# Kernel tuning notes

Measured on AMD Instinct MI355X. Metric: run time of the kernel, lower is better.

Reference implementation:

```python
import jax, jax.numpy as jnp
import numpy as np

N_HEADS = 8
EPS = 1e-6


def setup_inputs() -> dict:
    key = jax.random.key(0)
    k1, k2, k3, k4, k5 = jax.random.split(key, 5)
    C_in, C_out = 512, 512
    x = jax.random.normal(k1, (4, C_in, 128, 128), dtype=jnp.float32)
    # Linear layers: torch stores weight as (out, in); init ~ U(-1/sqrt(in), 1/sqrt(in))
    s_in = 1.0 / np.sqrt(C_in)
    w_qkv = jax.random.uniform(k2, (3 * C_in, C_in), minval=-s_in, maxval=s_in, dtype=jnp.float32)
    b_qkv = jax.random.uniform(k3, (3 * C_in,), minval=-s_in, maxval=s_in, dtype=jnp.float32)
    w_out = jax.random.uniform(k4, (C_out, C_in), minval=-s_in, maxval=s_in, dtype=jnp.float32)
    b_out = jax.random.uniform(k5, (C_out,), minval=-s_in, maxval=s_in, dtype=jnp.float32)
    return {"x": x, "w_qkv": w_qkv, "b_qkv": b_qkv, "w_out": w_out, "b_out": b_out}


def reference(x, w_qkv, b_qkv, w_out, b_out):
    B, C = x.shape[0], x.shape[1]
    spatial = x.shape[2:]
    c = C // N_HEADS  # channels per head
    # features_last=False: move channels to last, flatten spatial -> (B, N, C)
    xl = jnp.moveaxis(x, 1, -1).reshape(B, -1, C)
    N = xl.shape[1]
    qkv = xl @ w_qkv.T + b_qkv  # (B, N, 3*C)
    # einops '(qkv head channels)': qkv outermost, then head, then channels
    qkv = qkv.reshape(B, N, 3, N_HEADS, c)
    q = jax.nn.relu(qkv[:, :, 0])  # (B, N, H, c)
    k = jax.nn.relu(qkv[:, :, 1])
    v = qkv[:, :, 2]
    # Associativity: value @ key^T @ query == value @ (key^T @ query).
    # kq[b,h,c,d] = sum_n k[b,n,h,c] * q[b,n,h,d]  -> small (c x c) per head
    kq = jnp.einsum('bnhc,bnhd->bhcd', k, q)
    vkq = jnp.einsum('bnhc,bhcd->bnhd', v, kq)  # (B, N, H, c)
    # Padded ones-row of value corresponds to column-sum of kq over axis c
    norm = kq.sum(axis=2)[:, None] + EPS  # (B, 1, H, c)
    attn = vkq / norm  # (B, N, H, c)
    # torch: (B,H,N,c).moveaxis(1,-1) -> (B,N,c,H); flatten(-2) -> (B,N,c*H)
    attn = jnp.transpose(attn, (0, 1, 3, 2)).reshape(B, N, -1)
    out = attn @ w_out.T + b_out  # (B, N, C_out)
    out = out.reshape(B, *spatial, -1)
    out = jnp.moveaxis(out, -1, 1)  # (B, C_out, *spatial)
    return out
```

## Files before the change

### kernel.cpp

```cpp
#include <hip/hip_runtime.h>
#include <hip/hip_bf16.h>
#include <stdint.h>

#define NSP 16384
#define BATCH 4
#define EPSV 1e-6f

typedef __attribute__((ext_vector_type(8))) short fragAB;
typedef __attribute__((ext_vector_type(4))) float fragC;

__device__ __forceinline__ unsigned short f2bf(float f) {
    union { float f; unsigned u; } un; un.f = f;
    unsigned r = un.u + 0x7fffu + ((un.u >> 16) & 1u);
    return (unsigned short)(r >> 16);
}

__device__ __forceinline__ float bf2f(unsigned u) {
    union { unsigned u; float f; } x; x.u = u << 16; return x.f;
}

#define GLD_LDS(g, l) __builtin_amdgcn_global_load_lds( \
    (const __attribute__((address_space(1))) void*)(g), \
    (__attribute__((address_space(3))) void*)(l), 16, 0, 0)

__device__ __forceinline__ fragAB ldfrag(const unsigned short* ls, int m, int g) {
    return *(const fragAB*)&ls[((m >> 3) << 9) + ((m & 7) << 6) + ((g ^ (m & 7)) << 3)];
}

__device__ __forceinline__ int tidx(int ch, int g) {
    return (ch << 7) + ((g ^ (ch & 7)) << 3);
}

__global__ __launch_bounds__(256) void transpose_prep(
    const float* __restrict__ x, unsigned short* __restrict__ xt,
    const float* __restrict__ wqkv, unsigned short* __restrict__ wqb,
    unsigned short* __restrict__ wvT) {
    __shared__ float lds[64 * 65];
    const int blk = blockIdx.x;
    const int t   = threadIdx.x;
    if (blk < 8192) {
        const int b  = blk >> 11;
        const int c0 = ((blk >> 8) & 7) * 64;
        const int n0 = (blk & 255) * 64;
        const int nl = (t & 15) * 4;
        const int cl = t >> 4;
#pragma unroll
        for (int i = 0; i < 4; ++i) {
            int c = cl + i * 16;
            float4 v = *(const float4*)&x[((size_t)(b * 512 + c0 + c)) * NSP + n0 + nl];
            float* row = &lds[c * 65 + nl];
            row[0] = v.x; row[1] = v.y; row[2] = v.z; row[3] = v.w;
        }
        __syncthreads();
#pragma unroll
        for (int i = 0; i < 2; ++i) {
            int ch = t + i * 256;
            int n  = ch >> 3;
            int co = (ch & 7) * 8;
            unsigned v0, v1, v2, v3;
            v0 = f2bf(lds[(co + 0) * 65 + n]) | ((unsigned)f2bf(lds[(co + 1) * 65 + n]) << 16);
            v1 = f2bf(lds[(co + 2) * 65 + n]) | ((unsigned)f2bf(lds[(co + 3) * 65 + n]) << 16);
            v2 = f2bf(lds[(co + 4) * 65 + n]) | ((unsigned)f2bf(lds[(co + 5) * 65 + n]) << 16);
            v3 = f2bf(lds[(co + 6) * 65 + n]) | ((unsigned)f2bf(lds[(co + 7) * 65 + n]) << 16);
            uint4 pk; pk.x = v0; pk.y = v1; pk.z = v2; pk.w = v3;
            *(uint4*)&xt[((size_t)(b * NSP + n0 + n)) * 512 + c0 + co] = pk;
        }
        return;
    }
    const int pblk = blk - 8192;
    if (pblk < 512) {
        int i = (pblk * 256 + t) * 4;
        float4 v = *(const float4*)&wqkv[i];
        uint2 pk;
        pk.x = f2bf(v.x) | ((unsigned)f2bf(v.y) << 16);
        pk.y = f2bf(v.z) | ((unsigned)f2bf(v.w) << 16);
        *(uint2*)&wqb[i] = pk;
        return;
    }
    const int c0  = ((pblk - 512) & 7) * 64;
    const int ch0 = ((pblk - 512) >> 3) * 64;
    const int cl  = (t & 15) * 4;
    const int rl  = t >> 4;
#pragma unroll
    for (int i = 0; i < 4; ++i) {
        int r = rl + i * 16;
        float4 v = *(const float4*)&wqkv[((size_t)(1024 + ch0 + r)) * 512 + c0 + cl];
        float* row = &lds[r * 65 + cl];
        row[0] = v.x; row[1] = v.y; row[2] = v.z; row[3] = v.w;
    }
    __syncthreads();
#pragma unroll
    for (int i = 0; i < 2; ++i) {
        int idx = t + i * 256;
        int c = idx >> 3;
        int g = (idx & 7) * 8;
        unsigned v0, v1, v2, v3;
        v0 = f2bf(lds[(g + 0) * 65 + c]) | ((unsigned)f2bf(lds[(g + 1) * 65 + c]) << 16);
        v1 = f2bf(lds[(g + 2) * 65 + c]) | ((unsigned)f2bf(lds[(g + 3) * 65 + c]) << 16);
        v2 = f2bf(lds[(g + 4) * 65 + c]) | ((unsigned)f2bf(lds[(g + 5) * 65 + c]) << 16);
        v3 = f2bf(lds[(g + 6) * 65 + c]) | ((unsigned)f2bf(lds[(g + 7) * 65 + c]) << 16);
        uint4 pk; pk.x = v0; pk.y = v1; pk.z = v2; pk.w = v3;
        *(uint4*)&wvT[((size_t)(c0 + c)) * 512 + ch0 + g] = pk;
    }
}

__global__ __launch_bounds__(256, 2) void gemm_qk_kq(
    const unsigned short* __restrict__ xt, const unsigned short* __restrict__ wq,
    const float* __restrict__ bqkv, unsigned short* __restrict__ partb) {
    __shared__ unsigned short S[(128 + 256) * 64];
    __shared__ unsigned short Qt[128 * 128];
    unsigned short* Bls = &S[8192];
    unsigned short* Kt  = &S[0];

    const int b  = blockIdx.z;
    const int hc = blockIdx.y;
    const int bx = blockIdx.x;
    const int n0 = bx * 128;
    const int t  = threadIdx.x;
    const int wv = t >> 6, ln = t & 63;
    const unsigned short* Ag = xt + (size_t)(b * NSP + n0) * 512;
    const int srow = ln >> 3;
    const int scol = ((ln & 7) ^ srow) << 3;
    const int isK = wv >> 1;
    unsigned short* T = isK ? Kt : Qt;

    fragC acc[8][4];
#pragma unroll
    for (int i = 0; i < 8; ++i)
#pragma unroll
        for (int j = 0; j < 4; ++j) { acc[i][j][0]=0.f; acc[i][j][1]=0.f; acc[i][j][2]=0.f; acc[i][j][3]=0.f; }

    for (int k0 = 0; k0 < 512; k0 += 64) {
#pragma unroll
        for (int i = 0; i < 4; ++i) {
            int ca = wv * 4 + i;
            GLD_LDS(Ag + (size_t)(ca * 8 + srow) * 512 + k0 + scol, &S[ca * 512]);
        }
#pragma unroll
        for (int i = 0; i < 8; ++i) {
            int cb = wv * 8 + i;
            int jl = cb * 8 + srow;
            int rg = hc * 128 + jl + ((jl & 128) ? 384 : 0);
            GLD_LDS(wq + (size_t)rg * 512 + k0 + scol, &Bls[cb * 512]);
        }
        __syncthreads();
#pragma unroll
        for (int kk = 0; kk < 64; kk += 32) {
            int g = (kk >> 3) + (ln >> 4);
            fragAB bf[4];
#pragma unroll
            for (int nt = 0; nt < 4; ++nt) bf[nt] = ldfrag(Bls, wv * 64 + nt * 16 + (ln & 15), g);
#pragma unroll
            for (int mt = 0; mt < 8; ++mt) {
                fragAB a = ldfrag(S, mt * 16 + (ln & 15), g);
#pragma unroll
                for (int nt = 0; nt < 4; ++nt)
                    acc[mt][nt] = __builtin_amdgcn_mfma_f32_16x16x32_bf16(a, bf[nt], acc[mt][nt], 0, 0, 0);
            }
        }
        __syncthreads();
    }

#pragma unroll
    for (int nt = 0; nt < 4; ++nt) {
        int chl = (wv & 1) * 64 + nt * 16 + (ln & 15);
        float bias = bqkv[hc * 128 + chl + (isK ? 512 : 0)];
#pragma unroll
        for (int mt = 0; mt < 8; ++mt) {
            int nb = mt * 16 + (ln >> 4) * 4;
            float r0 = acc[mt][nt][0] + bias; r0 = r0 > 0.f ? r0 : 0.f;
            float r1 = acc[mt][nt][1] + bias; r1 = r1 > 0.f ? r1 : 0.f;
            float r2 = acc[mt][nt][2] + bias; r2 = r2 > 0.f ? r2 : 0.f;
            float r3 = acc[mt][nt][3] + bias; r3 = r3 > 0.f ? r3 : 0.f;
            uint2 pk;
            pk.x = f2bf(r0) | ((unsigned)f2bf(r1) << 16);
            pk.y = f2bf(r2) | ((unsigned)f2bf(r3) << 16);
            int g = nb >> 3, o = nb & 7;
            *(uint2*)&T[tidx(chl, g) + o] = pk;
        }
    }
    __syncthreads();

    {
        const int wm = wv >> 1, wn = wv & 1;
        fragC ak[2][4];
#pragma unroll
        for (int i = 0; i < 2; ++i)
#pragma unroll
            for (int j = 0; j < 4; ++j) { ak[i][j][0]=0.f; ak[i][j][1]=0.f; ak[i][j][2]=0.f; ak[i][j][3]=0.f; }
#pragma unroll
        for (int kk = 0; kk < 128; kk += 32) {
            int g = (kk >> 3) + (ln >> 4);
            fragAB qf[4];
#pragma unroll
            for (int dt = 0; dt < 4; ++dt)
                qf[dt] = *(const fragAB*)&Qt[tidx(wm * 64 + dt * 16 + (ln & 15), g)];
#pragma unroll
            for (int ct = 0; ct < 2; ++ct) {
                fragAB kf = *(const fragAB*)&Kt[tidx(wm * 64 + wn * 32 + ct * 16 + (ln & 15), g)];
#pragma unroll
                for (int dt = 0; dt < 4; ++dt)
                    ak[ct][dt] = __builtin_amdgcn_mfma_f32_16x16x32_bf16(qf[dt], kf, ak[ct][dt], 0, 0, 0);
            }
        }
        unsigned short* pb = partb + ((size_t)((b * 8 + hc * 2 + wm) * 128 + bx)) * 4096
                           + wn * 2048 + ln * 4;
#pragma unroll
        for (int ct = 0; ct < 2; ++ct)
#pragma unroll
            for (int dt = 0; dt < 4; ++dt) {
                uint2 pk;
                pk.x = f2bf(ak[ct][dt][0]) | ((unsigned)f2bf(ak[ct][dt][1]) << 16);
                pk.y = f2bf(ak[ct][dt][2]) | ((unsigned)f2bf(ak[ct][dt][3]) << 16);
                *(uint2*)&pb[ct * 1024 + dt * 256] = pk;
            }
    }
}

__global__ __launch_bounds__(256) void reduce_kq(const unsigned short* __restrict__ partb,
                                                 float* __restrict__ kq) {
    const int tid = blockIdx.x * 256 + threadIdx.x;
    const int bh  = tid >> 10;
    const int s   = tid & 1023;
    const int off = s * 4;
    const unsigned short* p = partb + (size_t)bh * 128 * 4096 + off;
    float s0 = 0.f, s1 = 0.f, s2 = 0.f, s3 = 0.f;
#pragma unroll 4
    for (int blk = 0; blk < 128; ++blk) {
        uint2 v = *(const uint2*)(p + (size_t)blk * 4096);
        s0 += bf2f(v.x & 0xffffu); s1 += bf2f(v.x >> 16);
        s2 += bf2f(v.y & 0xffffu); s3 += bf2f(v.y >> 16);
    }
    const int wn = off >> 11, ct = (off >> 10) & 1, dt = (off >> 8) & 3, ln = (off >> 2) & 63;
    const int c  = wn * 32 + ct * 16 + (ln & 15);
    const int d0 = dt * 16 + (ln >> 4) * 4;
    float4 o; o.x = s0; o.y = s1; o.z = s2; o.w = s3;
    *(float4*)&kq[(size_t)bh * 4096 + c * 64 + d0] = o;
}

__global__ __launch_bounds__(256) void w2_kernel(
    const float* __restrict__ kq, const float* __restrict__ wout,
    const float* __restrict__ bqkv,
    unsigned short* __restrict__ W2, float* __restrict__ b2ap) {
    __shared__ float slab[64 * 65];
    __shared__ float part[4 * 64];
    __shared__ float rnorm[64];
    __shared__ float wsc[32 * 65];
    const int jc = blockIdx.x;
    const int h  = blockIdx.y;
    const int b  = blockIdx.z;
    const int t  = threadIdx.x;
    const float* kqb = kq + ((size_t)(b * 8 + h)) * 4096;
#pragma unroll
    for (int i = 0; i < 4; ++i) {
        int e = t * 16 + i * 4;
        float4 v = *(const float4*)&kqb[e];
        float* r = &slab[(e >> 6) * 65 + (e & 63)];
        r[0] = v.x; r[1] = v.y; r[2] = v.z; r[3] = v.w;
    }
    __syncthreads();
    {
        int d = t & 63, cq = t >> 6;
        float s = 0.f;
        for (int c = cq * 16; c < cq * 16 + 16; ++c) s += slab[c * 65 + d];
        part[cq * 64 + d] = s;
    }
    __syncthreads();
    if (t < 64) rnorm[t] = 1.0f / (part[t] + part[64 + t] + part[128 + t] + part[192 + t] + EPSV);
    __syncthreads();
    {
        int jl = t >> 3;
        const float* wrow = &wout[((size_t)(jc * 32 + jl)) * 512 + h];
#pragma unroll
        for (int i = 0; i < 8; ++i) {
            int d = (t & 7) * 8 + i;
            wsc[jl * 65 + d] = wrow[d * 8] * rnorm[d];
        }
    }
    __syncthreads();
    {
        int jl = t >> 3, cg = (t & 7) * 8;
        int j  = jc * 32 + jl;
        float a[8] = {0.f, 0.f, 0.f, 0.f, 0.f, 0.f, 0.f, 0.f};
        for (int d = 0; d < 64; ++d) {
            float w = wsc[jl * 65 + d];
#pragma unroll
            for (int i = 0; i < 8; ++i) a[i] += w * slab[(cg + i) * 65 + d];
        }
        uint4 pk;
        pk.x = f2bf(a[0]) | ((unsigned)f2bf(a[1]) << 16);
        pk.y = f2bf(a[2]) | ((unsigned)f2bf(a[3]) << 16);
        pk.z = f2bf(a[4]) | ((unsigned)f2bf(a[5]) << 16);
        pk.w = f2bf(a[6]) | ((unsigned)f2bf(a[7]) << 16);
        *(uint4*)&W2[((size_t)(b * 512 + j)) * 512 + h * 64 + cg] = pk;
        const float* bv = &bqkv[1024 + h * 64 + cg];
        float p = 0.f;
#pragma unroll
        for (int i = 0; i < 8; ++i) p += a[i] * bv[i];
        p += __shfl_down(p, 4, 64);
        p += __shfl_down(p, 2, 64);
        p += __shfl_down(p, 1, 64);
        if ((t & 7) == 0) b2ap[((size_t)(b * 8 + h) << 9) + j] = p;
    }
}

__global__ __launch_bounds__(256) void w3_kernel(
    const unsigned short* __restrict__ wvT, const unsigned short* __restrict__ W2,
    unsigned short* __restrict__ W3) {
    __shared__ unsigned short Als[64 * 64];
    __shared__ unsigned short Bls[64 * 64];
    const int b  = blockIdx.z;
    const int m0 = blockIdx.x * 64;
    const int n0 = blockIdx.y * 64;
    const int t  = threadIdx.x;
    const int wv = t >> 6, ln = t & 63;
    const unsigned short* Ag = wvT + (size_t)m0 * 512;
    const unsigned short* Bg = W2 + ((size_t)(b * 512 + n0)) * 512;

    fragC acc[2][2];
#pragma unroll
    for (int i = 0; i < 2; ++i)
#pragma unroll
        for (int j = 0; j < 2; ++j) { acc[i][j][0]=0.f; acc[i][j][1]=0.f; acc[i][j][2]=0.f; acc[i][j][3]=0.f; }

    const int mw = (wv >> 1) * 32, nw = (wv & 1) * 32;
    const int srow = ln >> 3;
    const int scol = ((ln & 7) ^ srow) << 3;

    for (int k0 = 0; k0 < 512; k0 += 64) {
#pragma unroll
        for (int i = 0; i < 2; ++i) {
            int chunk = wv * 2 + i;
            int row = chunk * 8 + srow;
            GLD_LDS(Ag + (size_t)row * 512 + k0 + scol, &Als[chunk * 512]);
            GLD_LDS(Bg + (size_t)row * 512 + k0 + scol, &Bls[chunk * 512]);
        }
        __syncthreads();
#pragma unroll
        for (int kk = 0; kk < 64; kk += 32) {
            int g = (kk >> 3) + (ln >> 4);
            fragAB a[2], bf[2];
#pragma unroll
            for (int mt = 0; mt < 2; ++mt) a[mt]  = ldfrag(Als, mw + mt * 16 + (ln & 15), g);
#pragma unroll
            for (int nt = 0; nt < 2; ++nt) bf[nt] = ldfrag(Bls, nw + nt * 16 + (ln & 15), g);
#pragma unroll
            for (int mt = 0; mt < 2; ++mt)
#pragma unroll
                for (int nt = 0; nt < 2; ++nt)
                    acc[mt][nt] = __builtin_amdgcn_mfma_f32_16x16x32_bf16(a[mt], bf[nt], acc[mt][nt], 0, 0, 0);
        }
        __syncthreads();
    }

#pragma unroll
    for (int mt = 0; mt < 2; ++mt)
#pragma unroll
        for (int nt = 0; nt < 2; ++nt) {
            int c = m0 + mw + mt * 16 + (ln >> 4) * 4;
            int j = n0 + nw + nt * 16 + (ln & 15);
            uint2 pk;
            pk.x = f2bf(acc[mt][nt][0]) | ((unsigned)f2bf(acc[mt][nt][1]) << 16);
            pk.y = f2bf(acc[mt][nt][2]) | ((unsigned)f2bf(acc[mt][nt][3]) << 16);
            *(uint2*)&W3[((size_t)(b * 512 + j)) * 512 + c] = pk;
        }
}

__global__ __launch_bounds__(256, 2) void gemm_out(
    const unsigned short* __restrict__ xt, const unsigned short* __restrict__ W3,
    const float* __restrict__ b2ap, const float* __restrict__ bout,
    float* __restrict__ out) {
    __shared__ unsigned short Als[128 * 64];
    __shared__ unsigned short Bls[256 * 64];
    const int b  = blockIdx.z;
    const int n0 = blockIdx.x * 128;
    const int j0 = blockIdx.y * 256;
    const int t  = threadIdx.x;
    const int wv = t >> 6, ln = t & 63;
    const unsigned short* Ag = xt + (size_t)(b * NSP + n0) * 512;
    const unsigned short* Bg = W3 + ((size_t)(b * 512 + j0)) * 512;

    fragC acc[8][4];
#pragma unroll
    for (int i = 0; i < 8; ++i)
#pragma unroll
        for (int j = 0; j < 4; ++j) { acc[i][j][0]=0.f; acc[i][j][1]=0.f; acc[i][j][2]=0.f; acc[i][j][3]=0.f; }

    const int srow = ln >> 3;
    const int scol = ((ln & 7) ^ srow) << 3;

    for (int k0 = 0; k0 < 512; k0 += 64) {
#pragma unroll
        for (int i = 0; i < 4; ++i) {
            int ca = wv * 4 + i;
            GLD_LDS(Ag + (size_t)(ca * 8 + srow) * 512 + k0 + scol, &Als[ca * 512]);
        }
#pragma unroll
        for (int i = 0; i < 8; ++i) {
            int cb = wv * 8 + i;
            GLD_LDS(Bg + (size_t)(cb * 8 + srow) * 512 + k0 + scol, &Bls[cb * 512]);
        }
        __syncthreads();
#pragma unroll
        for (int kk = 0; kk < 64; kk += 32) {
            int g = (kk >> 3) + (ln >> 4);
            fragAB bf[4];
#pragma unroll
            for (int nt = 0; nt < 4; ++nt) bf[nt] = ldfrag(Bls, wv * 64 + nt * 16 + (ln & 15), g);
#pragma unroll
            for (int mt = 0; mt < 8; ++mt) {
                fragAB a = ldfrag(Als, mt * 16 + (ln & 15), g);
#pragma unroll
                for (int nt = 0; nt < 4; ++nt)
                    acc[mt][nt] = __builtin_amdgcn_mfma_f32_16x16x32_bf16(a, bf[nt], acc[mt][nt], 0, 0, 0);
            }
        }
        __syncthreads();
    }

#pragma unroll
    for (int nt = 0; nt < 4; ++nt) {
        int j = j0 + wv * 64 + nt * 16 + (ln & 15);
        float bias = bout[j];
#pragma unroll
        for (int h = 0; h < 8; ++h) bias += b2ap[((size_t)(b * 8 + h) << 9) + j];
#pragma unroll
        for (int mt = 0; mt < 8; ++mt) {
            int n = n0 + mt * 16 + (ln >> 4) * 4;
            float4 v;
            v.x = acc[mt][nt][0] + bias;
            v.y = acc[mt][nt][1] + bias;
            v.z = acc[mt][nt][2] + bias;
            v.w = acc[mt][nt][3] + bias;
            *(float4*)&out[((size_t)(b * 512 + j)) * NSP + n] = v;
        }
    }
}

extern "C" void kernel_launch(void* const* d_in, const int* in_sizes, int n_in,
                              void* d_out, int out_size, void* d_ws, size_t ws_size,
                              hipStream_t stream) {
    const float* x    = (const float*)d_in[0];
    const float* wqkv = (const float*)d_in[1];
    const float* bqkv = (const float*)d_in[2];
    const float* wout = (const float*)d_in[3];
    const float* bout = (const float*)d_in[4];
    float* out = (float*)d_out;

    char* p = (char*)d_ws;
    unsigned short* xt    = (unsigned short*)p; p += (size_t)BATCH * NSP * 512 * 2;
    unsigned short* wqb   = (unsigned short*)p; p += (size_t)1024 * 512 * 2;
    unsigned short* wvT   = (unsigned short*)p; p += (size_t)512 * 512 * 2;
    unsigned short* partb = (unsigned short*)p; p += (size_t)32 * 128 * 4096 * 2;
    float*          kq    = (float*)p;          p += (size_t)BATCH * 32768 * 4;
    float*          b2ap  = (float*)p;          p += (size_t)BATCH * 8 * 512 * 4;
    unsigned short* W2    = (unsigned short*)p; p += (size_t)BATCH * 512 * 512 * 2;
    unsigned short* W3    = (unsigned short*)p; p += (size_t)BATCH * 512 * 512 * 2;

    transpose_prep<<<dim3(8768), 256, 0, stream>>>(x, xt, wqkv, wqb, wvT);
    gemm_qk_kq<<<dim3(128, 4, BATCH), 256, 0, stream>>>(xt, wqb, bqkv, partb);
    reduce_kq<<<dim3(128), 256, 0, stream>>>(partb, kq);
    w2_kernel<<<dim3(16, 8, BATCH), 256, 0, stream>>>(kq, wout, bqkv, W2, b2ap);
    w3_kernel<<<dim3(8, 8, BATCH), 256, 0, stream>>>(wvT, W2, W3);
    gemm_out<<<dim3(128, 2, BATCH), 256, 0, stream>>>(xt, W3, b2ap, bout, out);
}
```

Measured before the change: 390.2 us.

## Fuse W2 and W3 weight-folding kernels into one kernel via shared-memory W2

Merges w2_kernel and w3_kernel into a single w2w3 kernel. Each block computes a 32-row slice of W2 for all heads into LDS, then multiplies it by a 128-row slice of wvT to produce W3 directly, so W2 never round-trips through global memory and one launch is removed. The bias partials are now summed per head in-kernel, so gemm_out reads one bias value instead of eight. The kq MFMA operand roles are swapped, and reduce_kq now writes kq transposed with scalar stores to match. The cost is that each of the four cq blocks redundantly recomputes the W2 slice, and LDS use per block is much larger.

```diff
diff --git a/kernel.cpp b/kernel.cpp
--- a/kernel.cpp
+++ b/kernel.cpp
@@ -183,36 +183,37 @@
 
     {
         const int wm = wv >> 1, wn = wv & 1;
-        fragC ak[2][4];
-#pragma unroll
-        for (int i = 0; i < 2; ++i)
-#pragma unroll
-            for (int j = 0; j < 4; ++j) { ak[i][j][0]=0.f; ak[i][j][1]=0.f; ak[i][j][2]=0.f; ak[i][j][3]=0.f; }
+        fragC ak[4][2];
+#pragma unroll
+        for (int i = 0; i < 4; ++i)
+#pragma unroll
+            for (int j = 0; j < 2; ++j) { ak[i][j][0]=0.f; ak[i][j][1]=0.f; ak[i][j][2]=0.f; ak[i][j][3]=0.f; }
+        const int dh = wn * 32;
 #pragma unroll
         for (int kk = 0; kk < 128; kk += 32) {
             int g = (kk >> 3) + (ln >> 4);
-            fragAB qf[4];
-#pragma unroll
-            for (int dt = 0; dt < 4; ++dt)
-                qf[dt] = *(const fragAB*)&Qt[tidx(wm * 64 + dt * 16 + (ln & 15), g)];
-#pragma unroll
-            for (int ct = 0; ct < 2; ++ct) {
-                fragAB kf = *(const fragAB*)&Kt[tidx(wm * 64 + wn * 32 + ct * 16 + (ln & 15), g)];
-#pragma unroll
-                for (int dt = 0; dt < 4; ++dt)
-                    ak[ct][dt] = __builtin_amdgcn_mfma_f32_16x16x32_bf16(qf[dt], kf, ak[ct][dt], 0, 0, 0);
+            fragAB bq[2];
+#pragma unroll
+            for (int dt = 0; dt < 2; ++dt)
+                bq[dt] = *(const fragAB*)&Qt[tidx(wm * 64 + dh + dt * 16 + (ln & 15), g)];
+#pragma unroll
+            for (int mt = 0; mt < 4; ++mt) {
+                fragAB a = *(const fragAB*)&Kt[tidx(wm * 64 + mt * 16 + (ln & 15), g)];
+#pragma unroll
+                for (int dt = 0; dt < 2; ++dt)
+                    ak[mt][dt] = __builtin_amdgcn_mfma_f32_16x16x32_bf16(a, bq[dt], ak[mt][dt], 0, 0, 0);
             }
         }
         unsigned short* pb = partb + ((size_t)((b * 8 + hc * 2 + wm) * 128 + bx)) * 4096
                            + wn * 2048 + ln * 4;
 #pragma unroll
-        for (int ct = 0; ct < 2; ++ct)
-#pragma unroll
-            for (int dt = 0; dt < 4; ++dt) {
+        for (int mt = 0; mt < 4; ++mt)
+#pragma unroll
+            for (int dt = 0; dt < 2; ++dt) {
                 uint2 pk;
-                pk.x = f2bf(ak[ct][dt][0]) | ((unsigned)f2bf(ak[ct][dt][1]) << 16);
-                pk.y = f2bf(ak[ct][dt][2]) | ((unsigned)f2bf(ak[ct][dt][3]) << 16);
-                *(uint2*)&pb[ct * 1024 + dt * 256] = pk;
+                pk.x = f2bf(ak[mt][dt][0]) | ((unsigned)f2bf(ak[mt][dt][1]) << 16);
+                pk.y = f2bf(ak[mt][dt][2]) | ((unsigned)f2bf(ak[mt][dt][3]) << 16);
+                *(uint2*)&pb[dt * 1024 + mt * 256] = pk;
             }
     }
 }
@@ -231,144 +232,146 @@
         s0 += bf2f(v.x & 0xffffu); s1 += bf2f(v.x >> 16);
         s2 += bf2f(v.y & 0xffffu); s3 += bf2f(v.y >> 16);
     }
-    const int wn = off >> 11, ct = (off >> 10) & 1, dt = (off >> 8) & 3, ln = (off >> 2) & 63;
-    const int c  = wn * 32 + ct * 16 + (ln & 15);
-    const int d0 = dt * 16 + (ln >> 4) * 4;
-    float4 o; o.x = s0; o.y = s1; o.z = s2; o.w = s3;
-    *(float4*)&kq[(size_t)bh * 4096 + c * 64 + d0] = o;
-}
-
-__global__ __launch_bounds__(256) void w2_kernel(
+    const int wn = off >> 11, dt = (off >> 10) & 1, mt = (off >> 8) & 3, ln = (off >> 2) & 63;
+    const int d  = wn * 32 + dt * 16 + (ln & 15);
+    const int c0 = mt * 16 + (ln >> 4) * 4;
+    float* o = &kq[(size_t)bh * 4096 + d];
+    o[(c0 + 0) * 64] = s0;
+    o[(c0 + 1) * 64] = s1;
+    o[(c0 + 2) * 64] = s2;
+    o[(c0 + 3) * 64] = s3;
+}
+
+__global__ __launch_bounds__(256) void w2w3(
     const float* __restrict__ kq, const float* __restrict__ wout,
-    const float* __restrict__ bqkv,
-    unsigned short* __restrict__ W2, float* __restrict__ b2ap) {
+    const float* __restrict__ bqkv, const unsigned short* __restrict__ wvT,
+    unsigned short* __restrict__ W3, float* __restrict__ b2a) {
     __shared__ float slab[64 * 65];
-    __shared__ float part[4 * 64];
+    __shared__ float p4[4 * 64];
     __shared__ float rnorm[64];
     __shared__ float wsc[32 * 65];
+    __shared__ unsigned short W2loc[32 * 520];
+    __shared__ unsigned short Als[128 * 64];
     const int jc = blockIdx.x;
-    const int h  = blockIdx.y;
+    const int cq = blockIdx.y;
     const int b  = blockIdx.z;
     const int t  = threadIdx.x;
-    const float* kqb = kq + ((size_t)(b * 8 + h)) * 4096;
-#pragma unroll
-    for (int i = 0; i < 4; ++i) {
-        int e = t * 16 + i * 4;
-        float4 v = *(const float4*)&kqb[e];
-        float* r = &slab[(e >> 6) * 65 + (e & 63)];
-        r[0] = v.x; r[1] = v.y; r[2] = v.z; r[3] = v.w;
-    }
-    __syncthreads();
-    {
-        int d = t & 63, cq = t >> 6;
-        float s = 0.f;
-        for (int c = cq * 16; c < cq * 16 + 16; ++c) s += slab[c * 65 + d];
-        part[cq * 64 + d] = s;
-    }
-    __syncthreads();
-    if (t < 64) rnorm[t] = 1.0f / (part[t] + part[64 + t] + part[128 + t] + part[192 + t] + EPSV);
-    __syncthreads();
-    {
-        int jl = t >> 3;
-        const float* wrow = &wout[((size_t)(jc * 32 + jl)) * 512 + h];
-#pragma unroll
-        for (int i = 0; i < 8; ++i) {
-            int d = (t & 7) * 8 + i;
-            wsc[jl * 65 + d] = wrow[d * 8] * rnorm[d];
-        }
-    }
-    __syncthreads();
-    {
-        int jl = t >> 3, cg = (t & 7) * 8;
-        int j  = jc * 32 + jl;
-        float a[8] = {0.f, 0.f, 0.f, 0.f, 0.f, 0.f, 0.f, 0.f};
-        for (int d = 0; d < 64; ++d) {
-            float w = wsc[jl * 65 + d];
-#pragma unroll
-            for (int i = 0; i < 8; ++i) a[i] += w * slab[(cg + i) * 65 + d];
-        }
-        uint4 pk;
-        pk.x = f2bf(a[0]) | ((unsigned)f2bf(a[1]) << 16);
-        pk.y = f2bf(a[2]) | ((unsigned)f2bf(a[3]) << 16);
-        pk.z = f2bf(a[4]) | ((unsigned)f2bf(a[5]) << 16);
-        pk.w = f2bf(a[6]) | ((unsigned)f2bf(a[7]) << 16);
-        *(uint4*)&W2[((size_t)(b * 512 + j)) * 512 + h * 64 + cg] = pk;
-        const float* bv = &bqkv[1024 + h * 64 + cg];
-        float p = 0.f;
-#pragma unroll
-        for (int i = 0; i < 8; ++i) p += a[i] * bv[i];
+    const int jl = t >> 3, cg = (t & 7) * 8;
+    float pacc = 0.f;
+
+    for (int h = 0; h < 8; ++h) {
+        const float* kqb = kq + ((size_t)(b * 8 + h)) * 4096;
+#pragma unroll
+        for (int i = 0; i < 4; ++i) {
+            int e = t * 16 + i * 4;
+            float4 v = *(const float4*)&kqb[e];
+            float* r = &slab[(e >> 6) * 65 + (e & 63)];
+            r[0] = v.x; r[1] = v.y; r[2] = v.z; r[3] = v.w;
+        }
+        __syncthreads();
+        {
+            int d = t & 63, cqq = t >> 6;
+            float s = 0.f;
+            for (int c = cqq * 16; c < cqq * 16 + 16; ++c) s += slab[c * 65 + d];
+            p4[cqq * 64 + d] = s;
+        }
+        __syncthreads();
+        if (t < 64) rnorm[t] = 1.0f / (p4[t] + p4[64 + t] + p4[128 + t] + p4[192 + t] + EPSV);
+        __syncthreads();
+        {
+            const float* wrow = &wout[((size_t)(jc * 32 + jl)) * 512 + h];
+#pragma unroll
+            for (int i = 0; i < 8; ++i) {
+                int d = (t & 7) * 8 + i;
+                wsc[jl * 65 + d] = wrow[d * 8] * rnorm[d];
+            }
+        }
+        __syncthreads();
+        {
+            float a[8] = {0.f, 0.f, 0.f, 0.f, 0.f, 0.f, 0.f, 0.f};
+            for (int d = 0; d < 64; ++d) {
+                float w = wsc[jl * 65 + d];
+#pragma unroll
+                for (int i = 0; i < 8; ++i) a[i] += w * slab[(cg + i) * 65 + d];
+            }
+            uint4 pk;
+            pk.x = f2bf(a[0]) | ((unsigned)f2bf(a[1]) << 16);
+            pk.y = f2bf(a[2]) | ((unsigned)f2bf(a[3]) << 16);
+            pk.z = f2bf(a[4]) | ((unsigned)f2bf(a[5]) << 16);
+            pk.w = f2bf(a[6]) | ((unsigned)f2bf(a[7]) << 16);
+            *(uint4*)&W2loc[jl * 520 + h * 64 + cg] = pk;
+            const float* bv = &bqkv[1024 + h * 64 + cg];
+#pragma unroll
+            for (int i = 0; i < 8; ++i) pacc += a[i] * bv[i];
+        }
+        __syncthreads();
+    }
+
+    if (cq == 0) {
+        float p = pacc;
         p += __shfl_down(p, 4, 64);
         p += __shfl_down(p, 2, 64);
         p += __shfl_down(p, 1, 64);
-        if ((t & 7) == 0) b2ap[((size_t)(b * 8 + h) << 9) + j] = p;
-    }
-}
-
-__global__ __launch_bounds__(256) void w3_kernel(
-    const unsigned short* __restrict__ wvT, const unsigned short* __restrict__ W2,
-    unsigned short* __restrict__ W3) {
-    __shared__ unsigned short Als[64 * 64];
-    __shared__ unsigned short Bls[64 * 64];
-    const int b  = blockIdx.z;
-    const int m0 = blockIdx.x * 64;
-    const int n0 = blockIdx.y * 64;
-    const int t  = threadIdx.x;
-    const int wv = t >> 6, ln = t & 63;
-    const unsigned short* Ag = wvT + (size_t)m0 * 512;
-    const unsigned short* Bg = W2 + ((size_t)(b * 512 + n0)) * 512;
-
-    fragC acc[2][2];
-#pragma unroll
-    for (int i = 0; i < 2; ++i)
-#pragma unroll
-        for (int j = 0; j < 2; ++j) { acc[i][j][0]=0.f; acc[i][j][1]=0.f; acc[i][j][2]=0.f; acc[i][j][3]=0.f; }
-
-    const int mw = (wv >> 1) * 32, nw = (wv & 1) * 32;
-    const int srow = ln >> 3;
-    const int scol = ((ln & 7) ^ srow) << 3;
-
-    for (int k0 = 0; k0 < 512; k0 += 64) {
-#pragma unroll
-        for (int i = 0; i < 2; ++i) {
-            int chunk = wv * 2 + i;
-            int row = chunk * 8 + srow;
-            GLD_LDS(Ag + (size_t)row * 512 + k0 + scol, &Als[chunk * 512]);
-            GLD_LDS(Bg + (size_t)row * 512 + k0 + scol, &Bls[chunk * 512]);
-        }
-        __syncthreads();
-#pragma unroll
-        for (int kk = 0; kk < 64; kk += 32) {
-            int g = (kk >> 3) + (ln >> 4);
-            fragAB a[2], bf[2];
-#pragma unroll
-            for (int mt = 0; mt < 2; ++mt) a[mt]  = ldfrag(Als, mw + mt * 16 + (ln & 15), g);
-#pragma unroll
-            for (int nt = 0; nt < 2; ++nt) bf[nt] = ldfrag(Bls, nw + nt * 16 + (ln & 15), g);
-#pragma unroll
-            for (int mt = 0; mt < 2; ++mt)
+        if ((t & 7) == 0) b2a[b * 512 + jc * 32 + jl] = p;
+    }
+    __syncthreads();
+
+    {
+        const int wv = t >> 6, ln = t & 63;
+        const int mw = wv * 32;
+        const int srow = ln >> 3;
+        const int scol = ((ln & 7) ^ srow) << 3;
+        const unsigned short* Ag = wvT + (size_t)(cq * 128) * 512;
+        fragC acc[2][2];
+#pragma unroll
+        for (int i = 0; i < 2; ++i)
+#pragma unroll
+            for (int j = 0; j < 2; ++j) { acc[i][j][0]=0.f; acc[i][j][1]=0.f; acc[i][j][2]=0.f; acc[i][j][3]=0.f; }
+
+        for (int k0 = 0; k0 < 512; k0 += 64) {
+#pragma unroll
+            for (int i = 0; i < 4; ++i) {
+                int chunk = wv * 4 + i;
+                int row = chunk * 8 + srow;
+                GLD_LDS(Ag + (size_t)row * 512 + k0 + scol, &Als[chunk * 512]);
+            }
+            __syncthreads();
+#pragma unroll
+            for (int kk = 0; kk < 64; kk += 32) {
+                int g = (kk >> 3) + (ln >> 4);
+                int koff = k0 + kk + (ln >> 4) * 8;
+                fragAB a[2], bf[2];
+#pragma unroll
+                for (int mt = 0; mt < 2; ++mt) a[mt] = ldfrag(Als, mw + mt * 16 + (ln & 15), g);
 #pragma unroll
                 for (int nt = 0; nt < 2; ++nt)
-                    acc[mt][nt] = __builtin_amdgcn_mfma_f32_16x16x32_bf16(a[mt], bf[nt], acc[mt][nt], 0, 0, 0);
-        }
-        __syncthreads();
-    }
-
-#pragma unroll
-    for (int mt = 0; mt < 2; ++mt)
-#pragma unroll
-        for (int nt = 0; nt < 2; ++nt) {
-            int c = m0 + mw + mt * 16 + (ln >> 4) * 4;
-            int j = n0 + nw + nt * 16 + (ln & 15);
-            uint2 pk;
-            pk.x = f2bf(acc[mt][nt][0]) | ((unsigned)f2bf(acc[mt][nt][1]) << 16);
-            pk.y = f2bf(acc[mt][nt][2]) | ((unsigned)f2bf(acc[mt][nt][3]) << 16);
-            *(uint2*)&W3[((size_t)(b * 512 + j)) * 512 + c] = pk;
-        }
+                    bf[nt] = *(const fragAB*)&W2loc[(nt * 16 + (ln & 15)) * 520 + koff];
+#pragma unroll
+                for (int mt = 0; mt < 2; ++mt)
+#pragma unroll
+                    for (int nt = 0; nt < 2; ++nt)
+                        acc[mt][nt] = __builtin_amdgcn_mfma_f32_16x16x32_bf16(a[mt], bf[nt], acc[mt][nt], 0, 0, 0);
+            }
+            __syncthreads();
+        }
+
+#pragma unroll
+        for (int mt = 0; mt < 2; ++mt)
+#pragma unroll
+            for (int nt = 0; nt < 2; ++nt) {
+                int c = cq * 128 + mw + mt * 16 + (ln >> 4) * 4;
+                int j = jc * 32 + nt * 16 + (ln & 15);
+                uint2 pk;
+                pk.x = f2bf(acc[mt][nt][0]) | ((unsigned)f2bf(acc[mt][nt][1]) << 16);
+                pk.y = f2bf(acc[mt][nt][2]) | ((unsigned)f2bf(acc[mt][nt][3]) << 16);
+                *(uint2*)&W3[((size_t)(b * 512 + j)) * 512 + c] = pk;
+            }
+    }
 }
 
 __global__ __launch_bounds__(256, 2) void gemm_out(
     const unsigned short* __restrict__ xt, const unsigned short* __restrict__ W3,
-    const float* __restrict__ b2ap, const float* __restrict__ bout,
+    const float* __restrict__ b2a, const float* __restrict__ bout,
     float* __restrict__ out) {
     __shared__ unsigned short Als[128 * 64];
     __shared__ unsigned short Bls[256 * 64];
@@ -421,9 +424,7 @@
 #pragma unroll
     for (int nt = 0; nt < 4; ++nt) {
         int j = j0 + wv * 64 + nt * 16 + (ln & 15);
-        float bias = bout[j];
-#pragma unroll
-        for (int h = 0; h < 8; ++h) bias += b2ap[((size_t)(b * 8 + h) << 9) + j];
+        float bias = bout[j] + b2a[b * 512 + j];
 #pragma unroll
         for (int mt = 0; mt < 8; ++mt) {
             int n = n0 + mt * 16 + (ln >> 4) * 4;
@@ -453,14 +454,12 @@
     unsigned short* wvT   = (unsigned short*)p; p += (size_t)512 * 512 * 2;
     unsigned short* partb = (unsigned short*)p; p += (size_t)32 * 128 * 4096 * 2;
     float*          kq    = (float*)p;          p += (size_t)BATCH * 32768 * 4;
-    float*          b2ap  = (float*)p;          p += (size_t)BATCH * 8 * 512 * 4;
-    unsigned short* W2    = (unsigned short*)p; p += (size_t)BATCH * 512 * 512 * 2;
+    float*          b2a   = (float*)p;          p += (size_t)BATCH * 512 * 4;
     unsigned short* W3    = (unsigned short*)p; p += (size_t)BATCH * 512 * 512 * 2;
 
     transpose_prep<<<dim3(8768), 256, 0, stream>>>(x, xt, wqkv, wqb, wvT);
     gemm_qk_kq<<<dim3(128, 4, BATCH), 256, 0, stream>>>(xt, wqb, bqkv, partb);
     reduce_kq<<<dim3(128), 256, 0, stream>>>(partb, kq);
-    w2_kernel<<<dim3(16, 8, BATCH), 256, 0, stream>>>(kq, wout, bqkv, W2, b2ap);
-    w3_kernel<<<dim3(8, 8, BATCH), 256, 0, stream>>>(wvT, W2, W3);
-    gemm_out<<<dim3(128, 2, BATCH), 256, 0, stream>>>(xt, W3, b2ap, bout, out);
-}
+    w2w3<<<dim3(16, 4, BATCH), 256, 0, stream>>>(kq, wout, bqkv, wvT, W3, b2a);
+    gemm_out<<<dim3(128, 2, BATCH), 256, 0, stream>>>(xt, W3, b2a, bout, out);
+}
```

Result: slower. 411.8 us (+5.6%).
